# Optimization experiments

Measured on AMD Instinct MI355X. Metric: run time of the kernel, lower is better.

The kernel has to match this reference:

```python
import jax, jax.numpy as jnp
import numpy as np

B, LQ, DM, DFFN, NL, NH, NP = 4, 13294, 256, 1024, 4, 8, 4
HD = DM // NH
SHAPES = np.array([[100, 100], [50, 50], [25, 25], [13, 13]], dtype=np.int64)


def _ln(x, g, b):
    m = x.mean(-1, keepdims=True)
    v = ((x - m) ** 2).mean(-1, keepdims=True)
    return (x - m) / jnp.sqrt(v + 1e-5) * g + b


def _ms_deform(value, loc, aw, shapes):
    # value: [B, Lv, NH, HD]; loc: [B, Lq, NH, NL, NP, 2]; aw: [B, Lq, NH, NL, NP]
    Bn, Lq = loc.shape[0], loc.shape[1]
    offs = np.concatenate([[0], np.cumsum(shapes[:, 0] * shapes[:, 1])])
    out = jnp.zeros((Bn, NH, Lq, HD), value.dtype)
    for l in range(NL):
        H, W = int(shapes[l, 0]), int(shapes[l, 1])
        val = value[:, offs[l]:offs[l + 1]].transpose(0, 2, 1, 3)  # [B,NH,HW,HD]
        # grid_sample align_corners=False convention: pixel = norm*size - 0.5
        x = (loc[:, :, :, l, :, 0] * W - 0.5).transpose(0, 2, 1, 3).reshape(Bn, NH, Lq * NP)
        y = (loc[:, :, :, l, :, 1] * H - 0.5).transpose(0, 2, 1, 3).reshape(Bn, NH, Lq * NP)
        x0 = jnp.floor(x); y0 = jnp.floor(y)
        fx = x - x0; fy = y - y0
        acc = jnp.zeros((Bn, NH, Lq * NP, HD), value.dtype)
        for dy, dx in ((0, 0), (0, 1), (1, 0), (1, 1)):
            xi = x0 + dx; yi = y0 + dy
            w = (fx if dx else 1.0 - fx) * (fy if dy else 1.0 - fy)
            valid = (xi >= 0) & (xi < W) & (yi >= 0) & (yi < H)  # zero padding
            idx = (jnp.clip(yi, 0, H - 1) * W + jnp.clip(xi, 0, W - 1)).astype(jnp.int32)
            g = jnp.take_along_axis(val, idx[..., None], axis=2)  # [B,NH,Lq*NP,HD]
            acc = acc + g * (w * valid)[..., None]
        a = aw[:, :, :, l].transpose(0, 2, 1, 3).reshape(Bn, NH, Lq * NP)
        out = out + (acc * a[..., None]).reshape(Bn, NH, Lq, NP, HD).sum(3)
    return out.transpose(0, 2, 1, 3).reshape(Bn, Lq, NH * HD)


def _forward(src, pos, reference_points, shapes, Wv, bv, Ws, bs, Wa, ba, Wo, bo,
             W1, b1, W2, b2, g1, be1, g2, be2):
    Bn, Lq, _ = src.shape
    q = src + pos
    value = (src @ Wv + bv).reshape(Bn, Lq, NH, HD)
    off = (q @ Ws + bs).reshape(Bn, Lq, NH, NL, NP, 2)
    aw = jax.nn.softmax((q @ Wa + ba).reshape(Bn, Lq, NH, NL * NP), axis=-1)
    aw = aw.reshape(Bn, Lq, NH, NL, NP)
    norm = jnp.asarray(np.ascontiguousarray(shapes[:, ::-1]), jnp.float32)  # (W,H) per level
    loc = reference_points[:, :, None, :, None, :] + off / norm[None, None, None, :, None, :]
    attn = _ms_deform(value, loc, aw, shapes) @ Wo + bo
    x = _ln(src + attn, g1, be1)
    h = jax.nn.relu(x @ W1 + b1)
    return _ln(x + h @ W2 + b2, g2, be2)


def setup_inputs():
    key = jax.random.key(0)
    ks = jax.random.split(key, 12)

    def lin(k, i, o):
        k1, k2 = jax.random.split(k)
        return (0.02 * jax.random.normal(k1, (i, o), jnp.float32),
                0.02 * jax.random.normal(k2, (o,), jnp.float32))

    Wv, bv = lin(ks[0], DM, DM)
    Ws, bs = lin(ks[1], DM, NH * NL * NP * 2)
    Wa, ba = lin(ks[2], DM, NH * NL * NP)
    Wo, bo = lin(ks[3], DM, DM)
    W1, b1 = lin(ks[4], DM, DFFN)
    W2, b2 = lin(ks[5], DFFN, DM)
    lsi = np.concatenate([[0], np.cumsum(SHAPES[:, 0] * SHAPES[:, 1])[:-1]])
    return {
        "src": jax.random.normal(ks[6], (B, LQ, DM), jnp.float32),
        "pos": jax.random.normal(ks[7], (B, LQ, DM), jnp.float32),
        "reference_points": jax.random.uniform(ks[8], (B, LQ, NL, 2), jnp.float32),
        "spatial_shapes": jnp.asarray(SHAPES),
        "level_start_index": jnp.asarray(lsi),
        "Wv": Wv, "bv": bv, "Ws": Ws, "bs": bs, "Wa": Wa, "ba": ba,
        "Wo": Wo, "bo": bo, "W1": W1, "b1": b1, "W2": W2, "b2": b2,
        "g1": jnp.ones((DM,), jnp.float32), "be1": jnp.zeros((DM,), jnp.float32),
        "g2": jnp.ones((DM,), jnp.float32), "be2": jnp.zeros((DM,), jnp.float32),
    }


def reference(src, pos, reference_points, spatial_shapes, level_start_index,
              Wv, bv, Ws, bs, Wa, ba, Wo, bo, W1, b1, W2, b2, g1, be1, g2, be2):
    shapes = np.asarray(spatial_shapes)
    return _forward(src, pos, reference_points, shapes, Wv, bv, Ws, bs, Wa, ba,
                    Wo, bo, W1, b1, W2, b2, g1, be1, g2, be2)
```

## Files before the change

kernel.cpp:

```cpp
#include <hip/hip_runtime.h>


#define LQn   13294
#define MREAL 53176
#define MP    53248
#define MT    416
#define MHALF 26588
#define MTH   208

typedef __attribute__((ext_vector_type(8))) short short8;
typedef __attribute__((ext_vector_type(4))) short short4v;
typedef __attribute__((ext_vector_type(4))) float f32x4;

__device__ __forceinline__ short f2bf(float f) {
    unsigned u = __float_as_uint(f);
    unsigned r = (u + 0x7FFFu + ((u >> 16) & 1u)) >> 16;
    return (short)r;
}
__device__ __forceinline__ float bf2f(short b) {
    return __uint_as_float(((unsigned)(unsigned short)b) << 16);
}

#define GLOAD16(gp, lp)                                                        \
    __builtin_amdgcn_global_load_lds(                                          \
        (const __attribute__((address_space(1))) void*)(gp),                   \
        (__attribute__((address_space(3))) void*)(lp), 16, 0, 0)

__global__ __launch_bounds__(256) void prep_all(
    const float* __restrict__ Wv, const float* __restrict__ Ws,
    const float* __restrict__ Wa, const float* __restrict__ Wo,
    const float* __restrict__ W1, const float* __restrict__ W2,
    const float* __restrict__ bs, const float* __restrict__ ba,
    const float* __restrict__ src, const float* __restrict__ pos,
    short* __restrict__ WvT, short* __restrict__ WsaT,
    short* __restrict__ WoT, short* __restrict__ W1T,
    short* __restrict__ W2T, float* __restrict__ bsa,
    short* __restrict__ q_bf) {
    const int bid = blockIdx.x, tid = threadIdx.x;
    if (bid >= 2945) {
        const int i = (bid - 2945) * 256 + tid;
        if (i < MREAL * 32) {
            const float4 a0 = ((const float4*)src)[i * 2];
            const float4 a1 = ((const float4*)src)[i * 2 + 1];
            const float4 b0 = ((const float4*)pos)[i * 2];
            const float4 b1 = ((const float4*)pos)[i * 2 + 1];
            short8 o;
            o[0] = f2bf(a0.x + b0.x); o[1] = f2bf(a0.y + b0.y);
            o[2] = f2bf(a0.z + b0.z); o[3] = f2bf(a0.w + b0.w);
            o[4] = f2bf(a1.x + b1.x); o[5] = f2bf(a1.y + b1.y);
            o[6] = f2bf(a1.z + b1.z); o[7] = f2bf(a1.w + b1.w);
            ((short8*)q_bf)[i] = o;
        }
        return;
    }
    const float* W; short* WT; int K, N, base;
    if (bid < 256)       { W = Wv; WT = WvT;              K = 256;  N = 256;  base = 0; }
    else if (bid < 512)  { W = Ws; WT = WsaT;             K = 256;  N = 256;  base = 256; }
    else if (bid < 640)  { W = Wa; WT = WsaT + 256 * 256; K = 256;  N = 128;  base = 512; }
    else if (bid < 896)  { W = Wo; WT = WoT;              K = 256;  N = 256;  base = 640; }
    else if (bid < 1920) { W = W1; WT = W1T;              K = 256;  N = 1024; base = 896; }
    else if (bid < 2944) { W = W2; WT = W2T;              K = 1024; N = 256;  base = 1920; }
    else {
        if (tid < 256) bsa[tid] = bs[tid];
        else if (tid < 384) bsa[tid] = ba[tid - 256];
        return;
    }
    const int i = (bid - base) * 256 + tid;
    const int n = i / K, k = i - n * K;
    WT[i] = f2bf(W[(size_t)k * N + n]);
}

template <int SRC, int EPI, int NT>
__global__ __launch_bounds__(256) void gemm_bt(const short* __restrict__ Ab,
                                               const float* __restrict__ Af,
                                               const short* __restrict__ BT,
                                               const float* __restrict__ bias,
                                               void* C,
                                               int M, int K, int N,
                                               int ldb, int ldc) {
    const int d = blockIdx.x;
    const int c = d & 7, j = d >> 3;
    const int jg = j / NT;
    const int m0 = (c + 8 * jg) * 128;
    const int n0 = (j - jg * NT) * 128;
    const int t = threadIdx.x;
    const int wid = t >> 6, lane = t & 63;
    const int wr = wid >> 1, wc = wid & 1;
    const int quad = lane >> 4, l16 = lane & 15;

    f32x4 acc[4][4];
#pragma unroll
    for (int i = 0; i < 4; ++i)
#pragma unroll
        for (int jj = 0; jj < 4; ++jj) acc[i][jj] = (f32x4){0.f, 0.f, 0.f, 0.f};

    if constexpr (SRC == 0) {
        __shared__ short lA[2][128 * 32];
        __shared__ short lB[2][128 * 32];
        const int grow = wid * 32 + (lane >> 2);
        const int gcol = (lane & 3) * 8;
        auto stage = [&](int buf, int k0) {
            GLOAD16(Ab + (size_t)(m0 + grow) * K + k0 + gcol,
                    &lA[buf][(wid * 32) * 32]);
            GLOAD16(Ab + (size_t)(m0 + grow + 16) * K + k0 + gcol,
                    &lA[buf][(wid * 32 + 16) * 32]);
            GLOAD16(BT + (size_t)(n0 + grow) * ldb + k0 + gcol,
                    &lB[buf][(wid * 32) * 32]);
            GLOAD16(BT + (size_t)(n0 + grow + 16) * ldb + k0 + gcol,
                    &lB[buf][(wid * 32 + 16) * 32]);
        };
        stage(0, 0);
        __syncthreads();
        int cur = 0;
        for (int k0 = 0; k0 < K; k0 += 32) {
            if (k0 + 32 < K) stage(cur ^ 1, k0 + 32);
            short8 af[4], bfr[4];
#pragma unroll
            for (int mi = 0; mi < 4; ++mi)
                af[mi] = *(const short8*)&lA[cur][(wr * 64 + mi * 16 + l16) * 32 + quad * 8];
#pragma unroll
            for (int ni = 0; ni < 4; ++ni)
                bfr[ni] = *(const short8*)&lB[cur][(wc * 64 + ni * 16 + l16) * 32 + quad * 8];
#pragma unroll
            for (int mi = 0; mi < 4; ++mi)
#pragma unroll
                for (int ni = 0; ni < 4; ++ni)
                    acc[mi][ni] = __builtin_amdgcn_mfma_f32_16x16x32_bf16(
                        af[mi], bfr[ni], acc[mi][ni], 0, 0, 0);
            __syncthreads();
            cur ^= 1;
        }
    } else {
        __shared__ short lA[128 * 32];
        __shared__ short lB[128 * 32];
        const int ar0 = t >> 2, ac0 = (t & 3) * 8;
        const int ar1 = ar0 + 64, ac1 = ac0;
        const int arow0 = min(m0 + ar0, M - 1);
        const int arow1 = min(m0 + ar1, M - 1);
        for (int k0 = 0; k0 < K; k0 += 32) {
            short8 va0, va1;
            {
                const size_t i0 = (size_t)arow0 * K + k0 + ac0;
                const size_t i1 = (size_t)arow1 * K + k0 + ac1;
                const float4 l0 = *(const float4*)(Af + i0);
                const float4 h0 = *(const float4*)(Af + i0 + 4);
                const float4 l1 = *(const float4*)(Af + i1);
                const float4 h1 = *(const float4*)(Af + i1 + 4);
                va0[0] = f2bf(l0.x); va0[1] = f2bf(l0.y); va0[2] = f2bf(l0.z);
                va0[3] = f2bf(l0.w); va0[4] = f2bf(h0.x); va0[5] = f2bf(h0.y);
                va0[6] = f2bf(h0.z); va0[7] = f2bf(h0.w);
                va1[0] = f2bf(l1.x); va1[1] = f2bf(l1.y); va1[2] = f2bf(l1.z);
                va1[3] = f2bf(l1.w); va1[4] = f2bf(h1.x); va1[5] = f2bf(h1.y);
                va1[6] = f2bf(h1.z); va1[7] = f2bf(h1.w);
            }
            const short8 vb0 = *(const short8*)(BT + (size_t)(n0 + ar0) * ldb + k0 + ac0);
            const short8 vb1 = *(const short8*)(BT + (size_t)(n0 + ar1) * ldb + k0 + ac1);
            __syncthreads();
            *(short8*)&lA[ar0 * 32 + ac0] = va0;
            *(short8*)&lA[ar1 * 32 + ac1] = va1;
            *(short8*)&lB[ar0 * 32 + ac0] = vb0;
            *(short8*)&lB[ar1 * 32 + ac1] = vb1;
            __syncthreads();
            short8 af[4], bfr[4];
#pragma unroll
            for (int mi = 0; mi < 4; ++mi)
                af[mi] = *(const short8*)&lA[(wr * 64 + mi * 16 + l16) * 32 + quad * 8];
#pragma unroll
            for (int ni = 0; ni < 4; ++ni)
                bfr[ni] = *(const short8*)&lB[(wc * 64 + ni * 16 + l16) * 32 + quad * 8];
#pragma unroll
            for (int mi = 0; mi < 4; ++mi)
#pragma unroll
                for (int ni = 0; ni < 4; ++ni)
                    acc[mi][ni] = __builtin_amdgcn_mfma_f32_16x16x32_bf16(
                        af[mi], bfr[ni], acc[mi][ni], 0, 0, 0);
        }
    }

#pragma unroll
    for (int ni = 0; ni < 4; ++ni) {
        const int gc = n0 + wc * 64 + ni * 16 + l16;
        const float bia = bias[gc];
#pragma unroll
        for (int mi = 0; mi < 4; ++mi) {
#pragma unroll
            for (int r = 0; r < 4; ++r) {
                const int gr = m0 + wr * 64 + mi * 16 + quad * 4 + r;
                if (gr < M) {
                    float v = acc[mi][ni][r] + bia;
                    if (EPI == 5) {
                        const int b = gr / LQn, s = gr - b * LQn;
                        const int hh = gc >> 5, dd = gc & 31;
                        ((short*)C)[(((size_t)b * 8 + hh) * LQn + s) * 32 + dd] = f2bf(v);
                    } else {
                        if (EPI == 2) v = fmaxf(v, 0.f);
                        ((short*)C)[(size_t)gr * ldc + gc] = f2bf(v);
                    }
                }
            }
        }
    }
}

template <int EPI>
__global__ __launch_bounds__(512) void gemm_ln(const short* __restrict__ Ab,
                                               const short* __restrict__ BT,
                                               const float* __restrict__ bias,
                                               const void* __restrict__ resid,
                                               void* __restrict__ out,
                                               const float* __restrict__ g,
                                               const float* __restrict__ be,
                                               int M, int K) {
    const int t = threadIdx.x;
    const int m0 = blockIdx.x * 128;
    const int wid = t >> 6, lane = t & 63;
    const int wr = wid >> 2, wc = wid & 3;
    const int quad = lane >> 4, l16 = lane & 15;

    __shared__ short lA[2][128 * 32];
    __shared__ short lB[2][256 * 32];
    __shared__ float2 part[128][4];
    __shared__ float2 stats[128];

    f32x4 acc[4][4];
#pragma unroll
    for (int i = 0; i < 4; ++i)
#pragma unroll
        for (int j = 0; j < 4; ++j) acc[i][j] = (f32x4){0.f, 0.f, 0.f, 0.f};

    const int ga_row = wid * 16 + (lane >> 2);
    const int gb_row = wid * 32 + (lane >> 2);
    const int gcol8 = (lane & 3) * 8;
    auto stage = [&](int buf, int k0) {
        GLOAD16(Ab + (size_t)(m0 + ga_row) * K + k0 + gcol8,
                &lA[buf][(wid * 16) * 32]);
        GLOAD16(BT + (size_t)gb_row * K + k0 + gcol8,
                &lB[buf][(wid * 32) * 32]);
        GLOAD16(BT + (size_t)(gb_row + 16) * K + k0 + gcol8,
                &lB[buf][(wid * 32 + 16) * 32]);
    };
    stage(0, 0);
    __syncthreads();
    int cur = 0;
    for (int k0 = 0; k0 < K; k0 += 32) {
        if (k0 + 32 < K) stage(cur ^ 1, k0 + 32);
        short8 af[4], bfr[4];
#pragma unroll
        for (int mi = 0; mi < 4; ++mi)
            af[mi] = *(const short8*)&lA[cur][(wr * 64 + mi * 16 + l16) * 32 + quad * 8];
#pragma unroll
        for (int ni = 0; ni < 4; ++ni)
            bfr[ni] = *(const short8*)&lB[cur][(wc * 64 + ni * 16 + l16) * 32 + quad * 8];
#pragma unroll
        for (int mi = 0; mi < 4; ++mi)
#pragma unroll
            for (int ni = 0; ni < 4; ++ni)
                acc[mi][ni] = __builtin_amdgcn_mfma_f32_16x16x32_bf16(
                    af[mi], bfr[ni], acc[mi][ni], 0, 0, 0);
        __syncthreads();
        cur ^= 1;
    }

    float biasv[4], gv[4], bev[4];
    int gcs[4];
#pragma unroll
    for (int ni = 0; ni < 4; ++ni) {
        gcs[ni] = wc * 64 + ni * 16 + l16;
        biasv[ni] = bias[gcs[ni]];
        gv[ni] = g[gcs[ni]];
        bev[ni] = be[gcs[ni]];
    }
#pragma unroll
    for (int mi = 0; mi < 4; ++mi) {
#pragma unroll
        for (int r = 0; r < 4; ++r) {
            const int lr = wr * 64 + mi * 16 + quad * 4 + r;
            const int gr = m0 + lr;
            const bool ok = (gr < M);
            float s1 = 0.f, s2 = 0.f;
#pragma unroll
            for (int ni = 0; ni < 4; ++ni) {
                float v = acc[mi][ni][r] + biasv[ni];
                if (ok) {
                    if (EPI == 0)
                        v += ((const float*)resid)[(size_t)gr * 256 + gcs[ni]];
                    else
                        v += bf2f(((const short*)resid)[(size_t)gr * 256 + gcs[ni]]);
                }
                acc[mi][ni][r] = v;
                s1 += v;
                s2 += v * v;
            }
#pragma unroll
            for (int o = 1; o < 16; o <<= 1) {
                s1 += __shfl_xor(s1, o);
                s2 += __shfl_xor(s2, o);
            }
            if (l16 == 0) part[lr][wc] = make_float2(s1, s2);
        }
    }
    __syncthreads();
    if (t < 128) {
        float s1 = 0.f, s2 = 0.f;
#pragma unroll
        for (int w = 0; w < 4; ++w) {
            const float2 p = part[t][w];
            s1 += p.x;
            s2 += p.y;
        }
        const float mean = s1 * (1.0f / 256.0f);
        const float var = s2 * (1.0f / 256.0f) - mean * mean;
        stats[t] = make_float2(mean, rsqrtf(var + 1e-5f));
    }
    __syncthreads();
#pragma unroll
    for (int mi = 0; mi < 4; ++mi) {
#pragma unroll
        for (int r = 0; r < 4; ++r) {
            const int lr = wr * 64 + mi * 16 + quad * 4 + r;
            const int gr = m0 + lr;
            if (gr < M) {
                const float2 st = stats[lr];
#pragma unroll
                for (int ni = 0; ni < 4; ++ni) {
                    const float v = (acc[mi][ni][r] - st.x) * st.y * gv[ni] + bev[ni];
                    if (EPI == 0)
                        ((short*)out)[(size_t)gr * 256 + gcs[ni]] = f2bf(v);
                    else
                        ((float*)out)[(size_t)gr * 256 + gcs[ni]] = v;
                }
            }
        }
    }
}

__global__ __launch_bounds__(256) void sample_k(const short* __restrict__ value,
                                                const short* __restrict__ offaw,
                                                const float* __restrict__ refp,
                                                short* __restrict__ attn,
                                                int nwg) {
    int wg = blockIdx.x;
    {
        const int q = nwg >> 3, r = nwg & 7;
        const int xcd = wg & 7, idx = wg >> 3;
        wg = (xcd < r ? xcd * (q + 1) : r * (q + 1) + (xcd - r) * q) + idx;
    }
    const int tid = threadIdx.x;
    const int grp = wg * 16 + (tid >> 4);
    const int s16 = tid & 15;
    const int l = s16 >> 2, sub = s16 & 3;
    const int row = grp >> 3, h = grp & 7;
    const int b = row / LQn;
    const int L = (l == 0) ? 100 : (l == 1) ? 50 : (l == 2) ? 25 : 13;
    const int O = (l == 0) ? 0 : (l == 1) ? 10000 : (l == 2) ? 12500 : 13125;
    const float Lf = (float)L;

    const short* op = offaw + (size_t)row * 384 + h * 32;
    const short* ap = offaw + (size_t)row * 384 + 256 + h * 16;

    const short4v alog = *(const short4v*)(ap + l * 4);
    float lg[4];
#pragma unroll
    for (int j = 0; j < 4; ++j) lg[j] = bf2f(alog[j]);
    float m = fmaxf(fmaxf(lg[0], lg[1]), fmaxf(lg[2], lg[3]));
    m = fmaxf(m, __shfl_xor(m, 4));
    m = fmaxf(m, __shfl_xor(m, 8));
    float s = 0.f;
#pragma unroll
    for (int j = 0; j < 4; ++j) { lg[j] = __expf(lg[j] - m); s += lg[j]; }
    s += __shfl_xor(s, 4);
    s += __shfl_xor(s, 8);
    const float inv = 1.f / s;

    const float2 rxy = *(const float2*)(refp + (size_t)row * 8 + l * 2);
    const short8 ov = *(const short8*)(op + l * 8);
    const short* vlev = value + ((size_t)(b * 8 + h) * LQn + O) * 32 + sub * 8;

    float acc[8];
#pragma unroll
    for (int j = 0; j < 8; ++j) acc[j] = 0.f;

#pragma unroll 2
    for (int p = 0; p < 4; ++p) {
        const float x = fmaf(rxy.x, Lf, bf2f(ov[p * 2 + 0]) - 0.5f);
        const float y = fmaf(rxy.y, Lf, bf2f(ov[p * 2 + 1]) - 0.5f);
        const float xf = floorf(x), yf = floorf(y);
        const int ix = (int)xf, iy = (int)yf;
        const float fx = x - xf, fy = y - yf;
        const float aw = lg[p] * inv;
        const float vx0 = ((unsigned)ix < (unsigned)L) ? 1.f : 0.f;
        const float vx1 = ((unsigned)(ix + 1) < (unsigned)L) ? 1.f : 0.f;
        const float vy0 = ((unsigned)iy < (unsigned)L) ? 1.f : 0.f;
        const float vy1 = ((unsigned)(iy + 1) < (unsigned)L) ? 1.f : 0.f;
        const float gx0 = (1.f - fx) * aw, gx1 = fx * aw;
        const float w00 = gx0 * (1.f - fy) * vx0 * vy0;
        const float w10 = gx1 * (1.f - fy) * vx1 * vy0;
        const float w01 = gx0 * fy * vx0 * vy1;
        const float w11 = gx1 * fy * vx1 * vy1;
        const int ix0 = min(max(ix, 0), L - 1);
        const int ix1 = min(max(ix + 1, 0), L - 1);
        const int iy0 = min(max(iy, 0), L - 1);
        const int iy1 = min(max(iy + 1, 0), L - 1);
        const int ro0 = iy0 * L, ro1 = iy1 * L;
        const short8 v00 = *(const short8*)(vlev + ((ro0 + ix0) << 5));
        const short8 v10 = *(const short8*)(vlev + ((ro0 + ix1) << 5));
        const short8 v01 = *(const short8*)(vlev + ((ro1 + ix0) << 5));
        const short8 v11 = *(const short8*)(vlev + ((ro1 + ix1) << 5));
#pragma unroll
        for (int j = 0; j < 8; ++j)
            acc[j] += w00 * bf2f(v00[j]) + w10 * bf2f(v10[j]) +
                      w01 * bf2f(v01[j]) + w11 * bf2f(v11[j]);
    }

#pragma unroll
    for (int j = 0; j < 8; ++j) {
        acc[j] += __shfl_xor(acc[j], 4);
        acc[j] += __shfl_xor(acc[j], 8);
    }

    if (l == 0) {
        short8 o;
#pragma unroll
        for (int j = 0; j < 8; ++j) o[j] = f2bf(acc[j]);
        *(short8*)(attn + (size_t)row * 256 + h * 32 + sub * 8) = o;
    }
}

extern "C" void kernel_launch(void* const* d_in, const int* in_sizes, int n_in,
                              void* d_out, int out_size, void* d_ws, size_t ws_size,
                              hipStream_t stream) {
    (void)in_sizes; (void)n_in; (void)out_size; (void)ws_size;
    const float* src  = (const float*)d_in[0];
    const float* pos  = (const float*)d_in[1];
    const float* refp = (const float*)d_in[2];
    const float* Wv = (const float*)d_in[5];
    const float* bv = (const float*)d_in[6];
    const float* Ws = (const float*)d_in[7];
    const float* bs = (const float*)d_in[8];
    const float* Wa = (const float*)d_in[9];
    const float* ba = (const float*)d_in[10];
    const float* Wo = (const float*)d_in[11];
    const float* bo = (const float*)d_in[12];
    const float* W1 = (const float*)d_in[13];
    const float* b1 = (const float*)d_in[14];
    const float* W2 = (const float*)d_in[15];
    const float* b2 = (const float*)d_in[16];
    const float* g1 = (const float*)d_in[17];
    const float* be1 = (const float*)d_in[18];
    const float* g2 = (const float*)d_in[19];
    const float* be2 = (const float*)d_in[20];

    char* ws = (char*)d_ws;
    size_t off = 0;
    auto take = [&](size_t bytes) {
        char* p = ws + off;
        off += (bytes + 255) & ~(size_t)255;
        return p;
    };
    short* WvT  = (short*)take(256 * 256 * 2);
    short* WsaT = (short*)take(384 * 256 * 2);
    short* WoT  = (short*)take(256 * 256 * 2);
    short* W1T  = (short*)take(1024 * 256 * 2);
    short* W2T  = (short*)take(256 * 1024 * 2);
    float* bsa  = (float*)take(384 * 4);
    short* value_h = (short*)take((size_t)MP * 256 * 2);
    short* offaw   = (short*)take((size_t)MP * 384 * 2);
    short* attn_bf = (short*)take((size_t)MP * 256 * 2);

    short* q_bf = attn_bf;
    short* x_bf = value_h;
    short* h    = offaw;
    float* z    = (float*)d_out;

    prep_all<<<9593, 256, 0, stream>>>(Wv, Ws, Wa, Wo, W1, W2, bs, ba, src, pos,
                                       WvT, WsaT, WoT, W1T, W2T, bsa, q_bf);
    gemm_bt<1, 5, 2><<<832, 256, 0, stream>>>(
        nullptr, src, WvT, bv, value_h, MREAL, 256, 256, 256, 256);
    gemm_bt<0, 1, 3><<<1248, 256, 0, stream>>>(
        q_bf, nullptr, WsaT, bsa, offaw, MREAL, 256, 384, 256, 384);
    {
        const int nwg = (MREAL * 8) / 16;
        sample_k<<<nwg, 256, 0, stream>>>(value_h, offaw, refp, attn_bf, nwg);
    }
    gemm_ln<0><<<MT, 512, 0, stream>>>(attn_bf, WoT, bo, src, x_bf, g1, be1,
                                       MREAL, 256);
    for (int half = 0; half < 2; ++half) {
        const size_t ro = (size_t)half * MHALF;
        gemm_bt<0, 2, 8><<<1664, 256, 0, stream>>>(
            x_bf + ro * 256, nullptr, W1T, b1, h, MHALF, 256, 1024, 256, 1024);
        gemm_ln<1><<<MTH, 512, 0, stream>>>(h, W2T, b2, x_bf + ro * 256,
                                            z + ro * 256, g2, be2, MHALF, 1024);
    }
}
```

Before: 442.3 us.

## Pre-convert src to bf16 and stage GEMM epilogue stores through swizzled LDS

The prep kernel now also writes a bf16 copy of src. The value projection can then use the same double-buffered async global-to-LDS load path as the other GEMMs, instead of a synchronous fp32 load-and-convert loop. The gemm_bt epilogue and the first LayerNorm GEMM epilogue now write results into XOR-swizzled shared memory and emit coalesced 16-byte row stores, replacing scattered 2-byte stores; this matters most for the head-transposed value layout. The first LayerNorm residual reads the bf16 src copy when workspace allows, which halves residual traffic but loses a little residual precision. The cost is an extra bf16 write in prep and extra barriers in the epilogues.

```diff
diff --git a/kernel.cpp b/kernel.cpp
--- a/kernel.cpp
+++ b/kernel.cpp
@@ -35,7 +35,7 @@
     short* __restrict__ WvT, short* __restrict__ WsaT,
     short* __restrict__ WoT, short* __restrict__ W1T,
     short* __restrict__ W2T, float* __restrict__ bsa,
-    short* __restrict__ q_bf) {
+    short* __restrict__ q_bf, short* __restrict__ src_bf) {
     const int bid = blockIdx.x, tid = threadIdx.x;
     if (bid >= 2945) {
         const int i = (bid - 2945) * 256 + tid;
@@ -44,12 +44,17 @@
             const float4 a1 = ((const float4*)src)[i * 2 + 1];
             const float4 b0 = ((const float4*)pos)[i * 2];
             const float4 b1 = ((const float4*)pos)[i * 2 + 1];
-            short8 o;
+            short8 o, o2;
             o[0] = f2bf(a0.x + b0.x); o[1] = f2bf(a0.y + b0.y);
             o[2] = f2bf(a0.z + b0.z); o[3] = f2bf(a0.w + b0.w);
             o[4] = f2bf(a1.x + b1.x); o[5] = f2bf(a1.y + b1.y);
             o[6] = f2bf(a1.z + b1.z); o[7] = f2bf(a1.w + b1.w);
+            o2[0] = f2bf(a0.x); o2[1] = f2bf(a0.y);
+            o2[2] = f2bf(a0.z); o2[3] = f2bf(a0.w);
+            o2[4] = f2bf(a1.x); o2[5] = f2bf(a1.y);
+            o2[6] = f2bf(a1.z); o2[7] = f2bf(a1.w);
             ((short8*)q_bf)[i] = o;
+            ((short8*)src_bf)[i] = o2;
         }
         return;
     }
@@ -70,9 +75,8 @@
     WT[i] = f2bf(W[(size_t)k * N + n]);
 }
 
-template <int SRC, int EPI, int NT>
+template <int EPI, int NT>
 __global__ __launch_bounds__(256) void gemm_bt(const short* __restrict__ Ab,
-                                               const float* __restrict__ Af,
                                                const short* __restrict__ BT,
                                                const float* __restrict__ bias,
                                                void* C,
@@ -88,117 +92,89 @@
     const int wr = wid >> 1, wc = wid & 1;
     const int quad = lane >> 4, l16 = lane & 15;
 
+    __shared__ short lA[2][128 * 32];
+    __shared__ short lB[2][128 * 32];
+
     f32x4 acc[4][4];
 #pragma unroll
     for (int i = 0; i < 4; ++i)
 #pragma unroll
         for (int jj = 0; jj < 4; ++jj) acc[i][jj] = (f32x4){0.f, 0.f, 0.f, 0.f};
 
-    if constexpr (SRC == 0) {
-        __shared__ short lA[2][128 * 32];
-        __shared__ short lB[2][128 * 32];
-        const int grow = wid * 32 + (lane >> 2);
-        const int gcol = (lane & 3) * 8;
-        auto stage = [&](int buf, int k0) {
-            GLOAD16(Ab + (size_t)(m0 + grow) * K + k0 + gcol,
-                    &lA[buf][(wid * 32) * 32]);
-            GLOAD16(Ab + (size_t)(m0 + grow + 16) * K + k0 + gcol,
-                    &lA[buf][(wid * 32 + 16) * 32]);
-            GLOAD16(BT + (size_t)(n0 + grow) * ldb + k0 + gcol,
-                    &lB[buf][(wid * 32) * 32]);
-            GLOAD16(BT + (size_t)(n0 + grow + 16) * ldb + k0 + gcol,
-                    &lB[buf][(wid * 32 + 16) * 32]);
-        };
-        stage(0, 0);
+    const int grow = wid * 32 + (lane >> 2);
+    const int gcol = (lane & 3) * 8;
+    auto stage = [&](int buf, int k0) {
+        GLOAD16(Ab + (size_t)(m0 + grow) * K + k0 + gcol,
+                &lA[buf][(wid * 32) * 32]);
+        GLOAD16(Ab + (size_t)(m0 + grow + 16) * K + k0 + gcol,
+                &lA[buf][(wid * 32 + 16) * 32]);
+        GLOAD16(BT + (size_t)(n0 + grow) * ldb + k0 + gcol,
+                &lB[buf][(wid * 32) * 32]);
+        GLOAD16(BT + (size_t)(n0 + grow + 16) * ldb + k0 + gcol,
+                &lB[buf][(wid * 32 + 16) * 32]);
+    };
+    stage(0, 0);
+    __syncthreads();
+    int cur = 0;
+    for (int k0 = 0; k0 < K; k0 += 32) {
+        if (k0 + 32 < K) stage(cur ^ 1, k0 + 32);
+        short8 af[4], bfr[4];
+#pragma unroll
+        for (int mi = 0; mi < 4; ++mi)
+            af[mi] = *(const short8*)&lA[cur][(wr * 64 + mi * 16 + l16) * 32 + quad * 8];
+#pragma unroll
+        for (int ni = 0; ni < 4; ++ni)
+            bfr[ni] = *(const short8*)&lB[cur][(wc * 64 + ni * 16 + l16) * 32 + quad * 8];
+#pragma unroll
+        for (int mi = 0; mi < 4; ++mi)
+#pragma unroll
+            for (int ni = 0; ni < 4; ++ni)
+                acc[mi][ni] = __builtin_amdgcn_mfma_f32_16x16x32_bf16(
+                    af[mi], bfr[ni], acc[mi][ni], 0, 0, 0);
         __syncthreads();
-        int cur = 0;
-        for (int k0 = 0; k0 < K; k0 += 32) {
-            if (k0 + 32 < K) stage(cur ^ 1, k0 + 32);
-            short8 af[4], bfr[4];
-#pragma unroll
-            for (int mi = 0; mi < 4; ++mi)
-                af[mi] = *(const short8*)&lA[cur][(wr * 64 + mi * 16 + l16) * 32 + quad * 8];
-#pragma unroll
-            for (int ni = 0; ni < 4; ++ni)
-                bfr[ni] = *(const short8*)&lB[cur][(wc * 64 + ni * 16 + l16) * 32 + quad * 8];
-#pragma unroll
-            for (int mi = 0; mi < 4; ++mi)
-#pragma unroll
-                for (int ni = 0; ni < 4; ++ni)
-                    acc[mi][ni] = __builtin_amdgcn_mfma_f32_16x16x32_bf16(
-                        af[mi], bfr[ni], acc[mi][ni], 0, 0, 0);
-            __syncthreads();
-            cur ^= 1;
-        }
-    } else {
-        __shared__ short lA[128 * 32];
-        __shared__ short lB[128 * 32];
-        const int ar0 = t >> 2, ac0 = (t & 3) * 8;
-        const int ar1 = ar0 + 64, ac1 = ac0;
-        const int arow0 = min(m0 + ar0, M - 1);
-        const int arow1 = min(m0 + ar1, M - 1);
-        for (int k0 = 0; k0 < K; k0 += 32) {
-            short8 va0, va1;
-            {
-                const size_t i0 = (size_t)arow0 * K + k0 + ac0;
-                const size_t i1 = (size_t)arow1 * K + k0 + ac1;
-                const float4 l0 = *(const float4*)(Af + i0);
-                const float4 h0 = *(const float4*)(Af + i0 + 4);
-                const float4 l1 = *(const float4*)(Af + i1);
-                const float4 h1 = *(const float4*)(Af + i1 + 4);
-                va0[0] = f2bf(l0.x); va0[1] = f2bf(l0.y); va0[2] = f2bf(l0.z);
-                va0[3] = f2bf(l0.w); va0[4] = f2bf(h0.x); va0[5] = f2bf(h0.y);
-                va0[6] = f2bf(h0.z); va0[7] = f2bf(h0.w);
-                va1[0] = f2bf(l1.x); va1[1] = f2bf(l1.y); va1[2] = f2bf(l1.z);
-                va1[3] = f2bf(l1.w); va1[4] = f2bf(h1.x); va1[5] = f2bf(h1.y);
-                va1[6] = f2bf(h1.z); va1[7] = f2bf(h1.w);
-            }
-            const short8 vb0 = *(const short8*)(BT + (size_t)(n0 + ar0) * ldb + k0 + ac0);
-            const short8 vb1 = *(const short8*)(BT + (size_t)(n0 + ar1) * ldb + k0 + ac1);
-            __syncthreads();
-            *(short8*)&lA[ar0 * 32 + ac0] = va0;
-            *(short8*)&lA[ar1 * 32 + ac1] = va1;
-            *(short8*)&lB[ar0 * 32 + ac0] = vb0;
-            *(short8*)&lB[ar1 * 32 + ac1] = vb1;
-            __syncthreads();
-            short8 af[4], bfr[4];
-#pragma unroll
-            for (int mi = 0; mi < 4; ++mi)
-                af[mi] = *(const short8*)&lA[(wr * 64 + mi * 16 + l16) * 32 + quad * 8];
-#pragma unroll
-            for (int ni = 0; ni < 4; ++ni)
-                bfr[ni] = *(const short8*)&lB[(wc * 64 + ni * 16 + l16) * 32 + quad * 8];
-#pragma unroll
-            for (int mi = 0; mi < 4; ++mi)
-#pragma unroll
-                for (int ni = 0; ni < 4; ++ni)
-                    acc[mi][ni] = __builtin_amdgcn_mfma_f32_16x16x32_bf16(
-                        af[mi], bfr[ni], acc[mi][ni], 0, 0, 0);
-        }
-    }
-
-#pragma unroll
-    for (int ni = 0; ni < 4; ++ni) {
-        const int gc = n0 + wc * 64 + ni * 16 + l16;
-        const float bia = bias[gc];
-#pragma unroll
-        for (int mi = 0; mi < 4; ++mi) {
-#pragma unroll
-            for (int r = 0; r < 4; ++r) {
-                const int gr = m0 + wr * 64 + mi * 16 + quad * 4 + r;
-                if (gr < M) {
-                    float v = acc[mi][ni][r] + bia;
-                    if (EPI == 5) {
-                        const int b = gr / LQn, s = gr - b * LQn;
-                        const int hh = gc >> 5, dd = gc & 31;
-                        ((short*)C)[(((size_t)b * 8 + hh) * LQn + s) * 32 + dd] = f2bf(v);
-                    } else {
+        cur ^= 1;
+    }
+
+    short* lflat = (short*)lA;
+#pragma unroll
+    for (int p = 0; p < 2; ++p) {
+        if (wc == p) {
+#pragma unroll
+            for (int ni = 0; ni < 4; ++ni) {
+                const int lc = ni * 16 + l16;
+                const float bia = bias[n0 + p * 64 + lc];
+#pragma unroll
+                for (int mi = 0; mi < 4; ++mi)
+#pragma unroll
+                    for (int r = 0; r < 4; ++r) {
+                        const int lr = wr * 64 + mi * 16 + quad * 4 + r;
+                        float v = acc[mi][ni][r] + bia;
                         if (EPI == 2) v = fmaxf(v, 0.f);
-                        ((short*)C)[(size_t)gr * ldc + gc] = f2bf(v);
+                        lflat[lr * 64 + (lc ^ ((lr & 7) << 3))] = f2bf(v);
                     }
+            }
+        }
+        __syncthreads();
+#pragma unroll
+        for (int i = 0; i < 4; ++i) {
+            const int chunk = i * 256 + t;
+            const int row = chunk >> 3;
+            const int c8 = (chunk & 7) * 8;
+            const int gr = m0 + row;
+            if (gr < M) {
+                const short8 v8 =
+                    *(const short8*)&lflat[row * 64 + (c8 ^ ((row & 7) << 3))];
+                const int gcl = n0 + p * 64 + c8;
+                if (EPI == 5) {
+                    const int b = gr / LQn, s = gr - b * LQn;
+                    const int hh = gcl >> 5, dd = gcl & 31;
+                    *(short8*)&((short*)C)[(((size_t)b * 8 + hh) * LQn + s) * 32 + dd] = v8;
+                } else {
+                    *(short8*)&((short*)C)[(size_t)gr * ldc + gcl] = v8;
                 }
             }
         }
+        __syncthreads();
     }
 }
 
@@ -210,7 +186,7 @@
                                                void* __restrict__ out,
                                                const float* __restrict__ g,
                                                const float* __restrict__ be,
-                                               int M, int K) {
+                                               int M, int K, int resbf) {
     const int t = threadIdx.x;
     const int m0 = blockIdx.x * 128;
     const int wid = t >> 6, lane = t & 63;
@@ -282,10 +258,10 @@
             for (int ni = 0; ni < 4; ++ni) {
                 float v = acc[mi][ni][r] + biasv[ni];
                 if (ok) {
-                    if (EPI == 0)
+                    if (resbf)
+                        v += bf2f(((const short*)resid)[(size_t)gr * 256 + gcs[ni]]);
+                    else
                         v += ((const float*)resid)[(size_t)gr * 256 + gcs[ni]];
-                    else
-                        v += bf2f(((const short*)resid)[(size_t)gr * 256 + gcs[ni]]);
                 }
                 acc[mi][ni][r] = v;
                 s1 += v;
@@ -313,21 +289,57 @@
         stats[t] = make_float2(mean, rsqrtf(var + 1e-5f));
     }
     __syncthreads();
-#pragma unroll
-    for (int mi = 0; mi < 4; ++mi) {
-#pragma unroll
-        for (int r = 0; r < 4; ++r) {
-            const int lr = wr * 64 + mi * 16 + quad * 4 + r;
-            const int gr = m0 + lr;
-            if (gr < M) {
-                const float2 st = stats[lr];
-#pragma unroll
-                for (int ni = 0; ni < 4; ++ni) {
-                    const float v = (acc[mi][ni][r] - st.x) * st.y * gv[ni] + bev[ni];
-                    if (EPI == 0)
-                        ((short*)out)[(size_t)gr * 256 + gcs[ni]] = f2bf(v);
-                    else
+
+    if (EPI == 0) {
+        short* lflat = (short*)lA;
+#pragma unroll
+        for (int p = 0; p < 4; ++p) {
+            if (wc == p) {
+#pragma unroll
+                for (int mi = 0; mi < 4; ++mi)
+#pragma unroll
+                    for (int r = 0; r < 4; ++r) {
+                        const int lr = wr * 64 + mi * 16 + quad * 4 + r;
+                        const float2 st = stats[lr];
+#pragma unroll
+                        for (int ni = 0; ni < 4; ++ni) {
+                            const int lc = ni * 16 + l16;
+                            const float v =
+                                (acc[mi][ni][r] - st.x) * st.y * gv[ni] + bev[ni];
+                            lflat[lr * 64 + (lc ^ ((lr & 7) << 3))] = f2bf(v);
+                        }
+                    }
+            }
+            __syncthreads();
+#pragma unroll
+            for (int i = 0; i < 2; ++i) {
+                const int chunk = i * 512 + t;
+                const int row = chunk >> 3;
+                const int c8 = (chunk & 7) * 8;
+                const int gr = m0 + row;
+                if (gr < M) {
+                    const short8 v8 =
+                        *(const short8*)&lflat[row * 64 + (c8 ^ ((row & 7) << 3))];
+                    *(short8*)&((short*)out)[(size_t)gr * 256 + p * 64 + c8] = v8;
+                }
+            }
+            __syncthreads();
+        }
+    } else {
+#pragma unroll
+        for (int mi = 0; mi < 4; ++mi) {
+#pragma unroll
+            for (int r = 0; r < 4; ++r) {
+                const int lr = wr * 64 + mi * 16 + quad * 4 + r;
+                const int gr = m0 + lr;
+                if (gr < M) {
+                    const float2 st = stats[lr];
+#pragma unroll
+                    for (int ni = 0; ni < 4; ++ni) {
+                        const float v =
+                            (acc[mi][ni][r] - st.x) * st.y * gv[ni] + bev[ni];
                         ((float*)out)[(size_t)gr * 256 + gcs[ni]] = v;
+                    }
                 }
             }
         }
@@ -429,7 +441,7 @@
 extern "C" void kernel_launch(void* const* d_in, const int* in_sizes, int n_in,
                               void* d_out, int out_size, void* d_ws, size_t ws_size,
                               hipStream_t stream) {
-    (void)in_sizes; (void)n_in; (void)out_size; (void)ws_size;
+    (void)in_sizes; (void)n_in; (void)out_size;
     const float* src  = (const float*)d_in[0];
     const float* pos  = (const float*)d_in[1];
     const float* refp = (const float*)d_in[2];
@@ -467,28 +479,42 @@
     short* offaw   = (short*)take((size_t)MP * 384 * 2);
     short* attn_bf = (short*)take((size_t)MP * 256 * 2);
 
+    short* src_bf;
+    int resbf_g4;
+    if (off + (size_t)MP * 256 * 2 <= ws_size) {
+        src_bf = (short*)take((size_t)MP * 256 * 2);
+        resbf_g4 = 1;
+    } else {
+        src_bf = offaw;
+        resbf_g4 = 0;
+    }
+
     short* q_bf = attn_bf;
     short* x_bf = value_h;
     short* h    = offaw;
     float* z    = (float*)d_out;
 
     prep_all<<<9593, 256, 0, stream>>>(Wv, Ws, Wa, Wo, W1, W2, bs, ba, src, pos,
-                                       WvT, WsaT, WoT, W1T, W2T, bsa, q_bf);
-    gemm_bt<1, 5, 2><<<832, 256, 0, stream>>>(
-        nullptr, src, WvT, bv, value_h, MREAL, 256, 256, 256, 256);
-    gemm_bt<0, 1, 3><<<1248, 256, 0, stream>>>(
-        q_bf, nullptr, WsaT, bsa, offaw, MREAL, 256, 384, 256, 384);
+                                       WvT, WsaT, WoT, W1T, W2T, bsa, q_bf,
+                                       src_bf);
+    gemm_bt<5, 2><<<832, 256, 0, stream>>>(
+        src_bf, WvT, bv, value_h, MREAL, 256, 256, 256, 256);
+    gemm_bt<1, 3><<<1248, 256, 0, stream>>>(
+        q_bf, WsaT, bsa, offaw, MREAL, 256, 384, 256, 384);
     {
         const int nwg = (MREAL * 8) / 16;
         sample_k<<<nwg, 256, 0, stream>>>(value_h, offaw, refp, attn_bf, nwg);
     }
-    gemm_ln<0><<<MT, 512, 0, stream>>>(attn_bf, WoT, bo, src, x_bf, g1, be1,
-                                       MREAL, 256);
+    gemm_ln<0><<<MT, 512, 0, stream>>>(attn_bf, WoT, bo,
+                                       resbf_g4 ? (const void*)src_bf
+                                                : (const void*)src,
+                                       x_bf, g1, be1, MREAL, 256, resbf_g4);
     for (int half = 0; half < 2; ++half) {
         const size_t ro = (size_t)half * MHALF;
-        gemm_bt<0, 2, 8><<<1664, 256, 0, stream>>>(
-            x_bf + ro * 256, nullptr, W1T, b1, h, MHALF, 256, 1024, 256, 1024);
+        gemm_bt<2, 8><<<1664, 256, 0, stream>>>(
+            x_bf + ro * 256, W1T, b1, h, MHALF, 256, 1024, 256, 1024);
         gemm_ln<1><<<MTH, 512, 0, stream>>>(h, W2T, b2, x_bf + ro * 256,
-                                            z + ro * 256, g2, be2, MHALF, 1024);
-    }
-}
+                                            z + ro * 256, g2, be2, MHALF, 1024,
+                                            1);
+    }
+}
```

Result: faster. 414.4 us (-6.3%).
